# Optimization experiments

Measured on AMD Instinct MI355X. Metric: run time of the kernel, lower is better.

## Reference

```python
import jax, jax.numpy as jnp
import numpy as np

T, B, C, U = 4000, 64, 64, 200
NEG_INF = jnp.float32(-1e30)


def setup_inputs() -> dict:
    key = jax.random.key(0)
    k1, k2 = jax.random.split(key)
    inputs = jax.random.normal(k1, (T, B, C), dtype=jnp.float32)  # time-major logits
    targets = jax.random.randint(k2, (B, U), 0, C, dtype=jnp.int32)
    return {"inputs": inputs, "targets": targets}


def reference(inputs, targets):
    # Transducer.forward: transitions is None -> log_softmax over classes.
    log_probs = jax.nn.log_softmax(inputs, axis=-1)  # [T, B, C]
    # emit[t, b, u] = log_probs[t, b, targets[b, u]]
    b_idx = jnp.arange(B)[:, None]  # [B, 1]
    emit = log_probs[:, b_idx, targets]  # [T, B, U]

    # ASG-style monotone alignment forward DP (no blank, repeats collapse):
    # alpha[t, u] = emit[t, u] + logsumexp(alpha[t-1, u], alpha[t-1, u-1])
    alpha0 = jnp.full((B, U), NEG_INF, dtype=inputs.dtype).at[:, 0].set(emit[0, :, 0])

    def step(alpha, emit_t):
        shifted = jnp.concatenate(
            [jnp.full((B, 1), NEG_INF, dtype=alpha.dtype), alpha[:, :-1]], axis=1
        )
        return emit_t + jnp.logaddexp(alpha, shifted), None

    alpha_T, _ = jax.lax.scan(step, alpha0, emit[1:])  # scan over T-1 frames
    losses = -alpha_T[:, U - 1]  # negated forward score per sample
    return jnp.mean(losses)  # TransducerLossFunction returns torch.mean(loss)
```

## Files before the change

### kernel.cpp

```cpp
#include <hip/hip_runtime.h>

#define T_DIM 4000
#define B_DIM 64
#define C_DIM 64
#define U_DIM 200
#define LOG2E 1.4426950408889634f
#define LN2 0.6931471805599453f

#define PAIRS 2000
#define PB_BYTES (PAIRS * 800)
#define NSLOT 20

__device__ __forceinline__ float hw_exp2(float x) { return __builtin_amdgcn_exp2f(x); }
__device__ __forceinline__ float hw_log2(float x) { return __builtin_amdgcn_logf(x); }

template <int CTRL>
__device__ __forceinline__ int dpp_i(int x) {
    return __builtin_amdgcn_update_dpp(0, x, CTRL, 0xF, 0xF, true);
}
template <int CTRL>
__device__ __forceinline__ float dpp_f(float x) {
    return __uint_as_float((unsigned)dpp_i<CTRL>((int)__float_as_uint(x)));
}

__device__ __forceinline__ unsigned rne_bf16(float v) {
    unsigned b = __float_as_uint(v);
    return b + 0x7FFFu + ((b >> 16) & 1u);
}

__global__ __launch_bounds__(256) void prep_kernel(const float* __restrict__ in,
                                                   const int* __restrict__ tgt,
                                                   unsigned* __restrict__ eg,
                                                   float* __restrict__ out) {
    __shared__ float ex[16 * 8 * 68];
    __shared__ unsigned tgc[400];
    __shared__ float red[4];
    const int tid = threadIdx.x;
    const int bg = blockIdx.x & 7;
    const int tc = blockIdx.x >> 3;
    const int t0 = tc * 16, b0 = bg * 8;

    for (int o = tid; o < 400; o += 256) {
        int4 tv = ((const int4*)tgt)[bg * 400 + o];
        tgc[o] = (unsigned)(tv.x & 63) | ((unsigned)(tv.y & 63) << 8)
               | ((unsigned)(tv.z & 63) << 16) | ((unsigned)(tv.w & 63) << 24);
    }
    #pragma unroll
    for (int k = 0; k < 8; ++k) {
        int flat = k * 256 + tid;
        int t_l = flat >> 7, i = flat & 127, b_l = i >> 4, q = i & 15;
        float4 v = *(const float4*)(in + (size_t)(t0 + t_l) * 4096 + (b0 + b_l) * 64 + q * 4);
        float4 e;
        e.x = hw_exp2(v.x * LOG2E); e.y = hw_exp2(v.y * LOG2E);
        e.z = hw_exp2(v.z * LOG2E); e.w = hw_exp2(v.w * LOG2E);
        *(float4*)&ex[(t_l * 8 + b_l) * 68 + q * 4] = e;
    }
    __syncthreads();

    {
        float v = 0.0f;
        if (tid < 128) {
            const float4* p = (const float4*)&ex[tid * 68];
            float s = 0.0f;
            #pragma unroll
            for (int j = 0; j < 16; ++j) { float4 a = p[j]; s += (a.x + a.y) + (a.z + a.w); }
            v = hw_log2(s);
        }
        #pragma unroll
        for (int o = 32; o > 0; o >>= 1) v += __shfl_xor(v, o);
        if ((tid & 63) == 0) red[tid >> 6] = v;
    }

    for (int it = 0; it < 13; ++it) {
        int o = it * 256 + tid;
        if (o < 3200) {
            int l = o % 50;
            int rest = o / 50;
            int b_l = rest & 7, tp_l = rest >> 3;
            unsigned tw = tgc[b_l * 50 + l];
            int c0 = tw & 255, c1 = (tw >> 8) & 255, c2 = (tw >> 16) & 255, c3 = tw >> 24;
            const float* plo = &ex[(tp_l * 16 + b_l) * 68];
            const float* phi = plo + 8 * 68;
            uint4 w;
            w.x = (rne_bf16(plo[c0]) >> 16) | (rne_bf16(plo[c1]) & 0xFFFF0000u);
            w.y = (rne_bf16(plo[c2]) >> 16) | (rne_bf16(plo[c3]) & 0xFFFF0000u);
            w.z = (rne_bf16(phi[c0]) >> 16) | (rne_bf16(phi[c1]) & 0xFFFF0000u);
            w.w = (rne_bf16(phi[c2]) >> 16) | (rne_bf16(phi[c3]) & 0xFFFF0000u);
            *(uint4*)((char*)eg + (size_t)(b0 + b_l) * PB_BYTES
                      + (size_t)(tc * 8 + tp_l) * 800 + l * 16) = w;
        }
    }
    __syncthreads();
    if (tid == 0)
        atomicAdd(out, (red[0] + red[1] + red[2] + red[3]) * (LN2 / 64.0f));
}

struct ScanState { float A0, A1, A2, A3; int S, D; };

__device__ __forceinline__ void renorm(ScanState& st, int lane) {
    float m = fmaxf(fmaxf(st.A0, st.A1), fmaxf(st.A2, st.A3));
    int e = (int)((__float_as_uint(m) >> 23) & 0xFFu);
    int cand = st.S + e - 127;
    int snb = dpp_i<0x138>(st.S);
    if (lane == 0) snb = -(1 << 28);
    int snew = max(cand, snb);
    int k = st.S - snew;
    st.A0 = ldexpf(st.A0, k);
    st.A1 = ldexpf(st.A1, k);
    st.A2 = ldexpf(st.A2, k);
    st.A3 = ldexpf(st.A3, k);
    st.S = snew;
    st.D = min(dpp_i<0x138>(snew) - snew, 60);
}

__device__ __forceinline__ void step(ScanState& st, float e0, float e1, float e2, float e3) {
    float sh = ldexpf(dpp_f<0x138>(st.A3), st.D);
    sh = fminf(sh, 1.125899906842624e15f);
    float t0 = st.A0 + sh;
    float t1 = st.A1 + st.A0;
    float t2 = st.A2 + st.A1;
    float t3 = st.A3 + st.A2;
    st.A0 = e0 * t0; st.A1 = e1 * t1; st.A2 = e2 * t2; st.A3 = e3 * t3;
}

__device__ __forceinline__ void brenorm(ScanState& st) {
    float m = fmaxf(fmaxf(st.A0, st.A1), fmaxf(st.A2, st.A3));
    int e = (int)((__float_as_uint(m) >> 23) & 0xFFu);
    int cand = st.S + e - 127;
    int snb = dpp_i<0x130>(st.S);
    int snew = max(cand, snb);
    int k = st.S - snew;
    st.A0 = ldexpf(st.A0, k);
    st.A1 = ldexpf(st.A1, k);
    st.A2 = ldexpf(st.A2, k);
    st.A3 = ldexpf(st.A3, k);
    st.S = snew;
    st.D = min(dpp_i<0x130>(snew) - snew, 60);
}

__device__ __forceinline__ void bstep(ScanState& st, float e0, float e1, float e2, float e3) {
    float e4s = fminf(ldexpf(dpp_f<0x130>(e0), st.D), 1.125899906842624e15f);
    float b0n = dpp_f<0x130>(st.A0);
    float g0 = e0 * st.A0, g1 = e1 * st.A1, g2 = e2 * st.A2, g3 = e3 * st.A3;
    st.A0 = g0 + g1; st.A1 = g1 + g2; st.A2 = g2 + g3; st.A3 = g3 + e4s * b0n;
}

__device__ __forceinline__ ScanState scan_init(const float* in, const int* tgt, int lane, int b) {
    float v0 = in[b * 64 + (tgt[b * U_DIM] & 63)];
    ScanState st;
    st.A0 = (lane == 0) ? hw_exp2(v0 * LOG2E) : 0.0f;
    st.A1 = 0.0f; st.A2 = 0.0f; st.A3 = 0.0f;
    st.S = 0; st.D = 0;
    return st;
}

#define LO(x) __uint_as_float((x) << 16)
#define HI(x) __uint_as_float((x) & 0xFFFF0000u)

__global__ __launch_bounds__(128, 1) void scan2_kernel(const float* __restrict__ in,
                                                       const int* __restrict__ tgt,
                                                       const unsigned* __restrict__ eg,
                                                       float* __restrict__ out) {
    __shared__ float jb0[64], jb1[64], jb2[64], jb3[64];
    __shared__ int jsb[64];
    const int lane = threadIdx.x & 63;
    const int wv = threadIdx.x >> 6;
    const int b = blockIdx.x;
    const int lidx = (lane < 50) ? lane : 49;
    const char* egb = (const char*)eg + (size_t)b * PB_BYTES;

    ScanState st;
    if (wv == 1) {
        st.A0 = 0.0f; st.A1 = 0.0f; st.A2 = 0.0f;
        st.A3 = (lane == 49) ? 1.0f : 0.0f;
        st.S = 0; st.D = 0;
        int off = 1999 * 800 + lidx * 16;
        uint4 wb[NSLOT];
        #pragma unroll
        for (int j = 0; j < NSLOT; ++j) { wb[j] = *(const uint4*)(egb + off); off -= 800; }
        for (int k = 0; k < 49; ++k) {
            #pragma unroll
            for (int j = 0; j < NSLOT; ++j) {
                if ((j & 3) == 0) brenorm(st);
                uint4 w = wb[j];
                wb[j] = *(const uint4*)(egb + off); off -= 800;
                bstep(st, LO(w.z), HI(w.z), LO(w.w), HI(w.w));
                bstep(st, LO(w.x), HI(w.x), LO(w.y), HI(w.y));
            }
        }
        #pragma unroll
        for (int j = 0; j < NSLOT; ++j) {
            if ((j & 3) == 0) brenorm(st);
            uint4 w = wb[j];
            bstep(st, LO(w.z), HI(w.z), LO(w.w), HI(w.w));
            if (j < NSLOT - 1) bstep(st, LO(w.x), HI(w.x), LO(w.y), HI(w.y));
        }
        brenorm(st);
        jb0[lane] = st.A0; jb1[lane] = st.A1; jb2[lane] = st.A2; jb3[lane] = st.A3;
        jsb[lane] = st.S;
    } else {
        st = scan_init(in, tgt, lane, b);
        int off = 800 + lidx * 16;
        uint4 wb[NSLOT];
        #pragma unroll
        for (int j = 0; j < NSLOT; ++j) { wb[j] = *(const uint4*)(egb + off); off += 800; }
        uint2 h0 = *(const uint2*)(egb + lidx * 16 + 8);
        step(st, LO(h0.x), HI(h0.x), LO(h0.y), HI(h0.y));
        for (int k = 0; k < 49; ++k) {
            #pragma unroll
            for (int j = 0; j < NSLOT; ++j) {
                if ((j & 3) == 0) renorm(st, lane);
                uint4 w = wb[j];
                wb[j] = *(const uint4*)(egb + off); off += 800;
                step(st, LO(w.x), HI(w.x), LO(w.y), HI(w.y));
                step(st, LO(w.z), HI(w.z), LO(w.w), HI(w.w));
            }
        }
        #pragma unroll
        for (int j = 0; j < NSLOT; ++j) {
            if ((j & 3) == 0) renorm(st, lane);
            uint4 w = wb[j];
            step(st, LO(w.x), HI(w.x), LO(w.y), HI(w.y));
            if (j < NSLOT - 1) step(st, LO(w.z), HI(w.z), LO(w.w), HI(w.w));
        }
        renorm(st, lane);
    }
    __syncthreads();
    if (wv == 0) {
        float d = st.A0 * jb0[lane] + st.A1 * jb1[lane]
                + st.A2 * jb2[lane] + st.A3 * jb3[lane];
        float ll = (lane < 50) ? hw_log2(fmaxf(d, 1e-38f)) + (float)(st.S + jsb[lane])
                               : -1e30f;
        float mx = ll;
        #pragma unroll
        for (int o = 32; o > 0; o >>= 1) mx = fmaxf(mx, __shfl_xor(mx, o));
        float s = (lane < 50) ? hw_exp2(ll - mx) : 0.0f;
        #pragma unroll
        for (int o = 32; o > 0; o >>= 1) s += __shfl_xor(s, o);
        if (lane == 0) atomicAdd(out, -(mx + hw_log2(s)) * (LN2 / 64.0f));
    }
}

__global__ __launch_bounds__(256) void lse_sum_kernel(const float* __restrict__ in,
                                                      float* __restrict__ out) {
    const int lane = threadIdx.x & 63;
    const int w = threadIdx.x >> 6;
    const int wid = blockIdx.x * 4 + w;
    const int ROWS = (T_DIM * B_DIM) / 1024;
    const float* p = in + (size_t)wid * ROWS * 64 + lane;
    float acc = 0.0f;
    for (int i = 0; i < ROWS; i += 2) {
        float xa = p[(size_t)i * 64];
        float xb = p[(size_t)(i + 1) * 64];
        float ea = hw_exp2(xa * LOG2E);
        float eb = hw_exp2(xb * LOG2E);
        #pragma unroll
        for (int off = 32; off > 0; off >>= 1) {
            ea += __shfl_xor(ea, off);
            eb += __shfl_xor(eb, off);
        }
        acc += hw_log2(ea) + hw_log2(eb);
    }
    __shared__ float red[4];
    if (lane == 0) red[w] = acc;
    __syncthreads();
    if (threadIdx.x == 0)
        atomicAdd(out, (red[0] + red[1] + red[2] + red[3]) * (LN2 / 64.0f));
}

__global__ __launch_bounds__(64) void scan_fb(const float* __restrict__ in,
                                              const int* __restrict__ tgt,
                                              float* __restrict__ out) {
    const int lane = threadIdx.x;
    const int b = blockIdx.x;
    const int lidx = (lane < 50) ? lane : 49;
    int4 tg = ((const int4*)(tgt + b * U_DIM))[lidx];
    tg.x &= 63; tg.y &= 63; tg.z &= 63; tg.w &= 63;
    ScanState st = scan_init(in, tgt, lane, b);
    const char* inb = (const char*)in;
    int o0 = 16384 + b * 256 + tg.x * 4;
    int o1 = 16384 + b * 256 + tg.y * 4;
    int o2 = 16384 + b * 256 + tg.z * 4;
    int o3 = 16384 + b * 256 + tg.w * 4;
    const int m0 = 3999 * 16384 + b * 256 + tg.x * 4;
    const int m1 = m0 + (tg.y - tg.x) * 4;
    const int m2 = m0 + (tg.z - tg.x) * 4;
    const int m3 = m0 + (tg.w - tg.x) * 4;
    float f0[16], f1[16], f2[16], f3[16];
    #pragma unroll
    for (int j = 0; j < 16; ++j) {
        f0[j] = *(const float*)(inb + min(o0, m0)); o0 += 16384;
        f1[j] = *(const float*)(inb + min(o1, m1)); o1 += 16384;
        f2[j] = *(const float*)(inb + min(o2, m2)); o2 += 16384;
        f3[j] = *(const float*)(inb + min(o3, m3)); o3 += 16384;
    }
    for (int k = 0; k < 249; ++k) {
        #pragma unroll
        for (int j = 0; j < 16; ++j) {
            if (j == 0 || j == 8) renorm(st, lane);
            float e0 = hw_exp2(f0[j] * LOG2E);
            float e1 = hw_exp2(f1[j] * LOG2E);
            float e2 = hw_exp2(f2[j] * LOG2E);
            float e3 = hw_exp2(f3[j] * LOG2E);
            f0[j] = *(const float*)(inb + min(o0, m0)); o0 += 16384;
            f1[j] = *(const float*)(inb + min(o1, m1)); o1 += 16384;
            f2[j] = *(const float*)(inb + min(o2, m2)); o2 += 16384;
            f3[j] = *(const float*)(inb + min(o3, m3)); o3 += 16384;
            step(st, e0, e1, e2, e3);
        }
    }
    #pragma unroll
    for (int j = 0; j < 15; ++j) {
        if (j == 0 || j == 8) renorm(st, lane);
        float e0 = hw_exp2(f0[j] * LOG2E);
        float e1 = hw_exp2(f1[j] * LOG2E);
        float e2 = hw_exp2(f2[j] * LOG2E);
        float e3 = hw_exp2(f3[j] * LOG2E);
        step(st, e0, e1, e2, e3);
    }
    if (lane == 49) {
        float a2 = hw_log2(fmaxf(st.A3, 1e-38f)) + (float)st.S;
        atomicAdd(out, -a2 * (LN2 / 64.0f));
    }
}

extern "C" void kernel_launch(void* const* d_in, const int* in_sizes, int n_in,
                              void* d_out, int out_size, void* d_ws, size_t ws_size,
                              hipStream_t stream) {
    const float* inputs = (const float*)d_in[0];
    const int* targets = (const int*)d_in[1];
    float* out = (float*)d_out;

    (void)hipMemsetAsync(out, 0, sizeof(float), stream);

    const size_t eg_bytes = (size_t)B_DIM * PB_BYTES;
    if (ws_size >= eg_bytes) {
        unsigned* eg = (unsigned*)d_ws;
        prep_kernel<<<2000, 256, 0, stream>>>(inputs, targets, eg, out);
        scan2_kernel<<<B_DIM, 128, 0, stream>>>(inputs, targets, eg, out);
    } else {
        scan_fb<<<B_DIM, 64, 0, stream>>>(inputs, targets, out);
        lse_sum_kernel<<<256, 256, 0, stream>>>(inputs, out);
    }
}
```

Before: 186.9 us.

## Precompute two-step transfer coefficients so each scan iteration applies a fused frame pair

The precompute kernel now stores the products of consecutive frames' emission probabilities, including the diagonal-shift term, in place of raw per-frame values. Forward and backward scans can then advance two frames in one fused update (fstep2/bstep2), which shortens the serial dependency chain per pair. Boundary frames are handled by reading raw logits directly. The cost is slightly more arithmetic per step, more DPP shuffles, and bf16 rounding applied to products instead of individual factors, which can change numerical accuracy.

```diff
diff --git a/kernel.cpp b/kernel.cpp
--- a/kernel.cpp
+++ b/kernel.cpp
@@ -10,6 +10,7 @@
 #define PAIRS 2000
 #define PB_BYTES (PAIRS * 800)
 #define NSLOT 20
+#define CLAMP50 1.125899906842624e15f
 
 __device__ __forceinline__ float hw_exp2(float x) { return __builtin_amdgcn_exp2f(x); }
 __device__ __forceinline__ float hw_log2(float x) { return __builtin_amdgcn_logf(x); }
@@ -79,13 +80,16 @@
             int b_l = rest & 7, tp_l = rest >> 3;
             unsigned tw = tgc[b_l * 50 + l];
             int c0 = tw & 255, c1 = (tw >> 8) & 255, c2 = (tw >> 16) & 255, c3 = tw >> 24;
+            int cm1 = l ? (int)(tgc[b_l * 50 + l - 1] >> 24) : c0;
             const float* plo = &ex[(tp_l * 16 + b_l) * 68];
             const float* phi = plo + 8 * 68;
+            float a0 = plo[c0], a1 = plo[c1], a2 = plo[c2], a3 = plo[c3], am = plo[cm1];
+            float b0v = phi[c0], b1v = phi[c1], b2v = phi[c2], b3v = phi[c3];
             uint4 w;
-            w.x = (rne_bf16(plo[c0]) >> 16) | (rne_bf16(plo[c1]) & 0xFFFF0000u);
-            w.y = (rne_bf16(plo[c2]) >> 16) | (rne_bf16(plo[c3]) & 0xFFFF0000u);
-            w.z = (rne_bf16(phi[c0]) >> 16) | (rne_bf16(phi[c1]) & 0xFFFF0000u);
-            w.w = (rne_bf16(phi[c2]) >> 16) | (rne_bf16(phi[c3]) & 0xFFFF0000u);
+            w.x = (rne_bf16(b0v * a0) >> 16) | (rne_bf16(b1v * a1) & 0xFFFF0000u);
+            w.y = (rne_bf16(b2v * a2) >> 16) | (rne_bf16(b3v * a3) & 0xFFFF0000u);
+            w.z = (rne_bf16(b0v * am) >> 16) | (rne_bf16(b1v * a0) & 0xFFFF0000u);
+            w.w = (rne_bf16(b2v * a1) >> 16) | (rne_bf16(b3v * a2) & 0xFFFF0000u);
             *(uint4*)((char*)eg + (size_t)(b0 + b_l) * PB_BYTES
                       + (size_t)(tc * 8 + tp_l) * 800 + l * 16) = w;
         }
@@ -115,7 +119,7 @@
 
 __device__ __forceinline__ void step(ScanState& st, float e0, float e1, float e2, float e3) {
     float sh = ldexpf(dpp_f<0x138>(st.A3), st.D);
-    sh = fminf(sh, 1.125899906842624e15f);
+    sh = fminf(sh, CLAMP50);
     float t0 = st.A0 + sh;
     float t1 = st.A1 + st.A0;
     float t2 = st.A2 + st.A1;
@@ -139,7 +143,7 @@
 }
 
 __device__ __forceinline__ void bstep(ScanState& st, float e0, float e1, float e2, float e3) {
-    float e4s = fminf(ldexpf(dpp_f<0x130>(e0), st.D), 1.125899906842624e15f);
+    float e4s = fminf(ldexpf(dpp_f<0x130>(e0), st.D), CLAMP50);
     float b0n = dpp_f<0x130>(st.A0);
     float g0 = e0 * st.A0, g1 = e1 * st.A1, g2 = e2 * st.A2, g3 = e3 * st.A3;
     st.A0 = g0 + g1; st.A1 = g1 + g2; st.A2 = g2 + g3; st.A3 = g3 + e4s * b0n;
@@ -156,6 +160,49 @@
 
 #define LO(x) __uint_as_float((x) << 16)
 #define HI(x) __uint_as_float((x) & 0xFFFF0000u)
+
+__device__ __forceinline__ void fstep2(ScanState& st, const uint4& w) {
+    float F0 = LO(w.x), F1 = HI(w.x), F2 = LO(w.y), F3 = HI(w.y);
+    float G0 = LO(w.z), G1 = HI(w.z), G2 = LO(w.w), G3 = HI(w.w);
+    float sh3 = fminf(ldexpf(dpp_f<0x138>(st.A3), st.D), CLAMP50);
+    float sh2 = fminf(ldexpf(dpp_f<0x138>(st.A2), st.D), CLAMP50);
+    float sm1 = sh3 + sh2;
+    float s0 = st.A0 + sh3;
+    float s1 = st.A1 + st.A0;
+    float s2 = st.A2 + st.A1;
+    float s3 = st.A3 + st.A2;
+    st.A0 = F0 * s0 + G0 * sm1;
+    st.A1 = F1 * s1 + G1 * s0;
+    st.A2 = F2 * s2 + G2 * s1;
+    st.A3 = F3 * s3 + G3 * s2;
+}
+
+__device__ __forceinline__ void bstep2(ScanState& st, const uint4& w) {
+    float F0 = LO(w.x), F1 = HI(w.x), F2 = LO(w.y), F3 = HI(w.y);
+    float G1 = HI(w.z), G2 = LO(w.w), G3 = HI(w.w);
+    float nF0 = dpp_f<0x130>(LO(w.x));
+    float nG0 = dpp_f<0x130>(LO(w.z));
+    float nG1 = dpp_f<0x130>(HI(w.z));
+    float nB0 = fminf(ldexpf(dpp_f<0x130>(st.A0), st.D), CLAMP50);
+    float nB1 = fminf(ldexpf(dpp_f<0x130>(st.A1), st.D), CLAMP50);
+    float H0 = F1 + G1, H1 = F2 + G2, H2 = F3 + G3, H3 = nF0 + nG0;
+    float n0 = F0 * st.A0 + H0 * st.A1 + G2 * st.A2;
+    float n1 = F1 * st.A1 + H1 * st.A2 + G3 * st.A3;
+    float n2 = F2 * st.A2 + H2 * st.A3 + nG0 * nB0;
+    float n3 = F3 * st.A3 + H3 * nB0  + nG1 * nB1;
+    st.A0 = n0; st.A1 = n1; st.A2 = n2; st.A3 = n3;
+}
+
+__device__ __forceinline__ float4 raw_e(const float* in, int b, int t,
+                                        int c0, int c1, int c2, int c3) {
+    const float* row = in + ((size_t)t * B_DIM + b) * C_DIM;
+    float4 e;
+    e.x = hw_exp2(row[c0] * LOG2E);
+    e.y = hw_exp2(row[c1] * LOG2E);
+    e.z = hw_exp2(row[c2] * LOG2E);
+    e.w = hw_exp2(row[c3] * LOG2E);
+    return e;
+}
 
 __global__ __launch_bounds__(128, 1) void scan2_kernel(const float* __restrict__ in,
                                                        const int* __restrict__ tgt,
@@ -169,6 +216,9 @@
     const int lidx = (lane < 50) ? lane : 49;
     const char* egb = (const char*)eg + (size_t)b * PB_BYTES;
 
+    int4 tg = ((const int4*)(tgt + b * U_DIM))[lidx];
+    tg.x &= 63; tg.y &= 63; tg.z &= 63; tg.w &= 63;
+
     ScanState st;
     if (wv == 1) {
         st.A0 = 0.0f; st.A1 = 0.0f; st.A2 = 0.0f;
@@ -184,44 +234,48 @@
                 if ((j & 3) == 0) brenorm(st);
                 uint4 w = wb[j];
                 wb[j] = *(const uint4*)(egb + off); off -= 800;
-                bstep(st, LO(w.z), HI(w.z), LO(w.w), HI(w.w));
-                bstep(st, LO(w.x), HI(w.x), LO(w.y), HI(w.y));
+                bstep2(st, w);
             }
         }
         #pragma unroll
-        for (int j = 0; j < NSLOT; ++j) {
+        for (int j = 0; j < NSLOT - 1; ++j) {
             if ((j & 3) == 0) brenorm(st);
-            uint4 w = wb[j];
-            bstep(st, LO(w.z), HI(w.z), LO(w.w), HI(w.w));
-            if (j < NSLOT - 1) bstep(st, LO(w.x), HI(w.x), LO(w.y), HI(w.y));
+            bstep2(st, wb[j]);
+        }
+        {
+            float4 e = raw_e(in, b, 2001, tg.x, tg.y, tg.z, tg.w);
+            bstep(st, e.x, e.y, e.z, e.w);
         }
         brenorm(st);
         jb0[lane] = st.A0; jb1[lane] = st.A1; jb2[lane] = st.A2; jb3[lane] = st.A3;
         jsb[lane] = st.S;
     } else {
         st = scan_init(in, tgt, lane, b);
+        {
+            float4 e = raw_e(in, b, 1, tg.x, tg.y, tg.z, tg.w);
+            step(st, e.x, e.y, e.z, e.w);
+        }
         int off = 800 + lidx * 16;
         uint4 wb[NSLOT];
         #pragma unroll
         for (int j = 0; j < NSLOT; ++j) { wb[j] = *(const uint4*)(egb + off); off += 800; }
-        uint2 h0 = *(const uint2*)(egb + lidx * 16 + 8);
-        step(st, LO(h0.x), HI(h0.x), LO(h0.y), HI(h0.y));
         for (int k = 0; k < 49; ++k) {
             #pragma unroll
             for (int j = 0; j < NSLOT; ++j) {
                 if ((j & 3) == 0) renorm(st, lane);
                 uint4 w = wb[j];
                 wb[j] = *(const uint4*)(egb + off); off += 800;
-                step(st, LO(w.x), HI(w.x), LO(w.y), HI(w.y));
-                step(st, LO(w.z), HI(w.z), LO(w.w), HI(w.w));
+                fstep2(st, w);
             }
         }
         #pragma unroll
-        for (int j = 0; j < NSLOT; ++j) {
+        for (int j = 0; j < NSLOT - 1; ++j) {
             if ((j & 3) == 0) renorm(st, lane);
-            uint4 w = wb[j];
-            step(st, LO(w.x), HI(w.x), LO(w.y), HI(w.y));
-            if (j < NSLOT - 1) step(st, LO(w.z), HI(w.z), LO(w.w), HI(w.w));
+            fstep2(st, wb[j]);
+        }
+        {
+            float4 e = raw_e(in, b, 2000, tg.x, tg.y, tg.z, tg.w);
+            step(st, e.x, e.y, e.z, e.w);
         }
         renorm(st, lane);
     }
```

Measured after the change: 196.2 us. 1.05x slower.
